# Kernel optimization log

Hardware: AMD Instinct MI355X
Metric: run time of the kernel (lower is better)

The kernel has to match this reference:

```python
import jax, jax.numpy as jnp
import numpy as np

BATCH, SEQ = 2, 2048
HID = 2048          # hidden_size
INTER = 4096        # intermediate_size
STATE = 16          # ssm_state_size
RANK = 128          # time_step_rank
K = 4               # conv_kernel


def setup_inputs() -> dict:
    key = jax.random.key(0)
    ks = jax.random.split(key, 8)
    s = 0.02
    return {
        "hidden_states": jax.random.normal(ks[0], (BATCH, SEQ, HID), jnp.float32),
        "in_proj_w": jax.random.normal(ks[1], (2 * INTER, HID), jnp.float32) * s,
        "conv_w": jax.random.normal(ks[2], (INTER, 1, K), jnp.float32) * s,   # depthwise (O, I/g=1, K)
        "conv_b": jnp.zeros((INTER,), jnp.float32),
        "x_proj_w": jax.random.normal(ks[3], (RANK + 2 * STATE, INTER), jnp.float32) * s,
        "dt_proj_w": jax.random.normal(ks[4], (INTER, RANK), jnp.float32) * s,
        "dt_proj_b": jax.random.normal(ks[5], (INTER,), jnp.float32) * s,
        "A_log": jnp.log(jnp.broadcast_to(jnp.arange(1, STATE + 1, dtype=jnp.float32), (INTER, STATE))),
        "D": jnp.ones((INTER,), jnp.float32),
        "out_proj_w": jax.random.normal(ks[6], (HID, INTER), jnp.float32) * s,
    }


def reference(hidden_states, in_proj_w, conv_w, conv_b, x_proj_w,
              dt_proj_w, dt_proj_b, A_log, D, out_proj_w):
    B, L, _ = hidden_states.shape
    # in_proj -> (B, L, 2*INTER), split into u (SSM input) and gate
    proj = jnp.einsum('blh,ph->blp', hidden_states, in_proj_w)
    u, gate = jnp.split(proj, 2, axis=-1)                       # (B, L, INTER) each
    # depthwise causal conv1d on channel-major layout (B, INTER, L)
    uc = jnp.swapaxes(u, 1, 2)
    conv = jax.lax.conv_general_dilated(
        uc, conv_w, window_strides=(1,), padding=[(K - 1, 0)],
        dimension_numbers=('NCH', 'OIH', 'NCH'), feature_group_count=INTER)
    u = jax.nn.silu(conv + conv_b[None, :, None])               # (B, INTER, L)
    # x_proj: dt-rank + B + C, computed in fp32 like the original
    ssm_p = jnp.einsum('bdl,pd->blp', u, x_proj_w).astype(jnp.float32)
    dt_r, Bm, Cm = jnp.split(ssm_p, [RANK, RANK + STATE], axis=-1)  # (B,L,RANK),(B,L,N),(B,L,N)
    dt = jax.nn.softplus(jnp.einsum('blr,dr->bld', dt_r, dt_proj_w) + dt_proj_b)  # (B, L, INTER)
    A = -jnp.exp(A_log)                                         # (INTER, STATE)

    def step(state, xs):
        dt_t, B_t, C_t, u_t = xs                                # (B,D),(B,N),(B,N),(B,D)
        dA = jnp.exp(dt_t[:, :, None] * A[None])                # (B, D, N)
        state = dA * state + (dt_t * u_t)[:, :, None] * B_t[:, None, :]
        y = jnp.einsum('bdn,bn->bd', state, C_t)
        return state, y

    xs = (jnp.swapaxes(dt, 0, 1),        # (L, B, D)
          jnp.swapaxes(Bm, 0, 1),        # (L, B, N)
          jnp.swapaxes(Cm, 0, 1),        # (L, B, N)
          jnp.moveaxis(u, 2, 0))         # (L, B, D)
    init = jnp.zeros((B, INTER, STATE), jnp.float32)
    _, ys = jax.lax.scan(step, init, xs)                        # (L, B, D)

    y = jnp.moveaxis(ys, 0, 1) + jnp.swapaxes(u, 1, 2) * D[None, None, :]  # skip connection
    y = y * jax.nn.silu(gate)
    return jnp.einsum('bld,hd->blh', y, out_proj_w)             # (B, L, HID)
```

## Files before the change

### kernel.cpp

```cpp
#include <hip/hip_runtime.h>

typedef unsigned int u32;
typedef unsigned short u16;
typedef float f32x4 __attribute__((ext_vector_type(4)));
typedef float f32x16 __attribute__((ext_vector_type(16)));
typedef u16 us4 __attribute__((ext_vector_type(4)));
typedef u16 us8 __attribute__((ext_vector_type(8)));
typedef __bf16 bf16x8 __attribute__((ext_vector_type(8)));

__device__ __forceinline__ u16 f2bf(float f) {
  u32 u = __builtin_bit_cast(u32, f);
  u += 0x7fffu + ((u >> 16) & 1u);
  return (u16)(u >> 16);
}
__device__ __forceinline__ float bf2f(u16 h) {
  u32 u = ((u32)h) << 16;
  return __builtin_bit_cast(float, u);
}
__device__ __forceinline__ void async16(const void* g, void* l) {
  __builtin_amdgcn_global_load_lds((const __attribute__((address_space(1))) void*)g,
                                   (__attribute__((address_space(3))) void*)l, 16, 0, 0);
}

template <int ACT, bool SPLITK = false>
__global__ __launch_bounds__(256) void gemm_bt(const u16* __restrict__ A,
                                               const u16* __restrict__ B,
                                               void* __restrict__ Cv,
                                               const float* __restrict__ bias,
                                               int K, int ldc) {
  __shared__ __align__(16) u16 As[128 * 64];
  __shared__ __align__(16) u16 Bs[128 * 64];
  const int tid = threadIdx.x;
  const int lane = tid & 63;
  const int wave = tid >> 6;
  const int ln = lane & 31;
  const int hw = lane >> 5;
  const int wm = (wave >> 1) << 6;
  const int wn = (wave & 1) << 6;
  const long rowBase = (long)blockIdx.y << 7;
  const long colBase = (long)blockIdx.x << 7;

  int kStart = 0, kEnd = K;
  if constexpr (SPLITK) {
    int kn = K / gridDim.z;
    kStart = blockIdx.z * kn;
    kEnd = kStart + kn;
  }

  const int rr = tid >> 3;
  const int qg = (tid & 7) ^ (rr & 7);
  const u16* Ag = A + (rowBase + rr) * (long)K + qg * 8;
  const u16* Bg = B + (colBase + rr) * (long)K + qg * 8;
  u16* Al = As + tid * 8;
  u16* Bl = Bs + tid * 8;

  f32x16 acc[2][2] = {};
  const int l7 = ln & 7;

  for (int k0 = kStart; k0 < kEnd; k0 += 64) {
#pragma unroll
    for (int c = 0; c < 4; ++c) {
      async16(Ag + 32L * c * K + k0, Al + 2048 * c);
      async16(Bg + 32L * c * K + k0, Bl + 2048 * c);
    }
    __syncthreads();
#pragma unroll
    for (int s = 0; s < 4; ++s) {
      const int xa = ((s * 2 + hw) ^ l7) * 8;
      us8 af[2], bfr[2];
#pragma unroll
      for (int i = 0; i < 2; ++i)
        af[i] = *(const us8*)(As + (wm + i * 32 + ln) * 64 + xa);
#pragma unroll
      for (int i = 0; i < 2; ++i)
        bfr[i] = *(const us8*)(Bs + (wn + i * 32 + ln) * 64 + xa);
#pragma unroll
      for (int i = 0; i < 2; ++i)
#pragma unroll
        for (int j = 0; j < 2; ++j)
          acc[i][j] = __builtin_amdgcn_mfma_f32_32x32x16_bf16(
              __builtin_bit_cast(bf16x8, af[i]), __builtin_bit_cast(bf16x8, bfr[j]),
              acc[i][j], 0, 0, 0);
    }
    __syncthreads();
  }

  float* Cf = (float*)Cv;
  if constexpr (SPLITK)
    Cf += (size_t)blockIdx.z * ((size_t)gridDim.y * 128 * ldc);

#pragma unroll
  for (int i = 0; i < 2; ++i)
#pragma unroll
    for (int j = 0; j < 2; ++j)
#pragma unroll
      for (int r = 0; r < 16; ++r) {
        long row = rowBase + wm + i * 32 + (r & 3) + 8 * (r >> 2) + 4 * hw;
        long col = colBase + wn + j * 32 + ln;
        float v = acc[i][j][r];
        if constexpr (ACT == 0) {
          Cf[row * ldc + col] = v;
        } else if constexpr (ACT == 1) {
          ((u16*)Cv)[row * ldc + col] = f2bf(v);
        } else if constexpr (ACT == 2) {
          float s = v / (1.f + __expf(-v));
          ((u16*)Cv)[row * ldc + col] = f2bf(s);
        } else if constexpr (ACT == 3) {
          v += bias[col];
          float sp = (v > 20.f) ? v : log1pf(__expf(v));
          Cf[row * ldc + col] = sp;
        } else if constexpr (ACT == 4) {
          v += bias[col];
          float sp = (v > 20.f) ? v : log1pf(__expf(v));
          ((u16*)Cv)[row * ldc + col] = f2bf(sp);
        } else {
          if (colBase < 4096) {
            ((u16*)Cv)[row * 4096 + col] = f2bf(v);
          } else {
            float s = v / (1.f + __expf(-v));
            ((u16*)(size_t)bias)[row * 4096 + (col - 4096)] = f2bf(s);
          }
        }
      }
}

__device__ __forceinline__ void cvt4(const float* __restrict__ in,
                                     u16* __restrict__ out, int i) {
  f32x4 v = ((const f32x4*)in)[i];
  us4 o;
  o[0] = f2bf(v[0]); o[1] = f2bf(v[1]); o[2] = f2bf(v[2]); o[3] = f2bf(v[3]);
  ((us4*)out)[i] = o;
}
__global__ __launch_bounds__(256) void cvt_all(
    const float* __restrict__ hs, const float* __restrict__ wIn,
    const float* __restrict__ wOut, const float* __restrict__ wDt,
    const float* __restrict__ wX, u16* __restrict__ Xb, u16* __restrict__ Winb,
    u16* __restrict__ Wob, u16* __restrict__ Wdtb, u16* __restrict__ Wxb) {
  int i = blockIdx.x * 256 + threadIdx.x;
  if (i < 2097152) { cvt4(hs, Xb, i); return; }
  i -= 2097152;
  if (i < 4194304) { cvt4(wIn, Winb, i); return; }
  i -= 4194304;
  if (i < 2097152) { cvt4(wOut, Wob, i); return; }
  i -= 2097152;
  if (i < 131072) { cvt4(wDt, Wdtb, i); return; }
  i -= 131072;
  if (i >= 262144) return;
  int row = (i << 2) >> 12;
  us4 o;
  if (row < 160) {
    f32x4 v = ((const f32x4*)wX)[i];
    o[0] = f2bf(v[0]); o[1] = f2bf(v[1]); o[2] = f2bf(v[2]); o[3] = f2bf(v[3]);
  } else {
    o[0] = 0; o[1] = 0; o[2] = 0; o[3] = 0;
  }
  ((us4*)Wxb)[i] = o;
}

__global__ __launch_bounds__(256) void xp_reduce(const float* __restrict__ part,
                                                 float* __restrict__ smp,
                                                 u16* __restrict__ dtrb) {
  int i = blockIdx.x * 256 + threadIdx.x;
  const f32x4* p = (const f32x4*)part;
  f32x4 v = p[i];
  v += p[i + 262144];
  v += p[i + 524288];
  v += p[i + 786432];
  ((f32x4*)smp)[i] = v;
  int e = i << 2;
  int c = e & 255;
  if (c < 128) {
    int t = e >> 8;
    us4 o;
    o[0] = f2bf(v[0]); o[1] = f2bf(v[1]); o[2] = f2bf(v[2]); o[3] = f2bf(v[3]);
    *(us4*)(dtrb + t * 128 + c) = o;
  }
}

__global__ __launch_bounds__(256) void conv_silu(const u16* __restrict__ U,
                                                 const float* __restrict__ cw,
                                                 const float* __restrict__ cb,
                                                 u16* __restrict__ out) {
  int i = blockIdx.x * 256 + threadIdx.x;
  int t = i >> 10;
  int d4 = (i & 1023) << 2;
  int l = t & 2047;
  float w[4][4];
#pragma unroll
  for (int j = 0; j < 4; ++j) {
    f32x4 wv = *(const f32x4*)(cw + (d4 + j) * 4);
    w[j][0] = wv[0]; w[j][1] = wv[1]; w[j][2] = wv[2]; w[j][3] = wv[3];
  }
  float r[4] = {cb[d4], cb[d4 + 1], cb[d4 + 2], cb[d4 + 3]};
#pragma unroll
  for (int k = 0; k < 4; ++k) {
    int ll = l - 3 + k;
    if (ll >= 0) {
      us4 xv = *(const us4*)(U + (size_t)(t - 3 + k) * 4096 + d4);
      r[0] += w[0][k] * bf2f(xv[0]);
      r[1] += w[1][k] * bf2f(xv[1]);
      r[2] += w[2][k] * bf2f(xv[2]);
      r[3] += w[3][k] * bf2f(xv[3]);
    }
  }
  us4 o;
#pragma unroll
  for (int j = 0; j < 4; ++j) {
    float v = r[j];
    float s = v / (1.f + __expf(-v));
    o[j] = f2bf(s);
  }
  *(us4*)(out + (size_t)t * 4096 + d4) = o;
}

__global__ __launch_bounds__(256) void scan_part(
    const u16* __restrict__ dt, const u16* __restrict__ ub,
    const float* __restrict__ ssmp, const float* __restrict__ Alog,
    float* __restrict__ Sout, float* __restrict__ dtsumo) {
  const int tid = threadIdx.x;
  const int chunk = blockIdx.x, dgrp = blockIdx.y, b = blockIdx.z;
  const int d = (dgrp << 8) + tid;
  float A[16];
#pragma unroll
  for (int q = 0; q < 4; ++q) {
    f32x4 v = *(const f32x4*)(Alog + d * 16 + q * 4);
    A[q * 4 + 0] = -__expf(v[0]);
    A[q * 4 + 1] = -__expf(v[1]);
    A[q * 4 + 2] = -__expf(v[2]);
    A[q * 4 + 3] = -__expf(v[3]);
  }
  bool fastl = true;
#pragma unroll
  for (int n = 1; n < 16; ++n)
    fastl = fastl && (fabsf(A[n] - (n + 1) * A[0]) <= 1e-4f * (float)(n + 1));
  const bool fast = (__ballot(fastl) == ~0ull);

  const int base = b * 2048 + chunk * 64;
  const u16* dtp = dt + (size_t)base * 4096 + d;
  const u16* up = ub + (size_t)base * 4096 + d;
  const float* Bp = ssmp + (size_t)base * 256 + 128;

  float s[16] = {};
  float dtsum = 0.f;
  float cdt[8], cu[8], ndt[8] = {}, nu[8] = {};
#pragma unroll
  for (int j = 0; j < 8; ++j) {
    cdt[j] = bf2f(dtp[j * 4096]);
    cu[j] = bf2f(up[j * 4096]);
  }
  for (int l0 = 0; l0 < 64; l0 += 8) {
    if (l0 + 8 < 64) {
      int o = (l0 + 8) * 4096;
#pragma unroll
      for (int j = 0; j < 8; ++j) {
        ndt[j] = bf2f(dtp[o + j * 4096]);
        nu[j] = bf2f(up[o + j * 4096]);
      }
    }
    if (fast) {
#pragma unroll
      for (int j = 0; j < 8; ++j) {
        float e1 = __expf(cdt[j] * A[0]);
        float x = cdt[j] * cu[j];
        const float* Bl = Bp + (l0 + j) * 256;
        f32x4 B0 = *(const f32x4*)(Bl);
        f32x4 B1 = *(const f32x4*)(Bl + 4);
        f32x4 B2 = *(const f32x4*)(Bl + 8);
        f32x4 B3 = *(const f32x4*)(Bl + 12);
        float p = 1.f;
#pragma unroll
        for (int n = 0; n < 16; ++n) {
          p *= e1;
          float Bn = (n < 4) ? B0[n & 3] : (n < 8) ? B1[n & 3] : (n < 12) ? B2[n & 3] : B3[n & 3];
          s[n] = fmaf(p, s[n], x * Bn);
        }
        dtsum += cdt[j];
      }
    } else {
#pragma unroll
      for (int j = 0; j < 8; ++j) {
        float x = cdt[j] * cu[j];
        const float* Bl = Bp + (l0 + j) * 256;
        f32x4 B0 = *(const f32x4*)(Bl);
        f32x4 B1 = *(const f32x4*)(Bl + 4);
        f32x4 B2 = *(const f32x4*)(Bl + 8);
        f32x4 B3 = *(const f32x4*)(Bl + 12);
#pragma unroll
        for (int n = 0; n < 16; ++n) {
          float e = __expf(cdt[j] * A[n]);
          float Bn = (n < 4) ? B0[n & 3] : (n < 8) ? B1[n & 3] : (n < 12) ? B2[n & 3] : B3[n & 3];
          s[n] = fmaf(e, s[n], x * Bn);
        }
        dtsum += cdt[j];
      }
    }
#pragma unroll
    for (int j = 0; j < 8; ++j) { cdt[j] = ndt[j]; cu[j] = nu[j]; }
  }
  size_t o = ((size_t)(b * 32 + chunk) * 16) * 4096 + d;
#pragma unroll
  for (int n = 0; n < 16; ++n) Sout[o + (size_t)n * 4096] = s[n];
  dtsumo[(size_t)(b * 32 + chunk) * 4096 + d] = dtsum;
}

__global__ __launch_bounds__(256) void scan_fold(
    const float* __restrict__ Sin, const float* __restrict__ dtsum,
    const float* __restrict__ Alog, float* __restrict__ Sinit) {
  const int tid = threadIdx.x;
  const int n = blockIdx.x, dgrp = blockIdx.y, b = blockIdx.z;
  const int d = (dgrp << 8) + tid;
  const float A = -__expf(Alog[d * 16 + n]);
  float run = 0.f;
  for (int c = 0; c < 32; ++c) {
    size_t o = ((size_t)(b * 32 + c) * 16 + n) * 4096 + d;
    Sinit[o] = run;
    float P = __expf(dtsum[(size_t)(b * 32 + c) * 4096 + d] * A);
    run = fmaf(P, run, Sin[o]);
  }
}

__global__ __launch_bounds__(256) void scan_y(
    const u16* __restrict__ dt, const u16* __restrict__ ub,
    const float* __restrict__ ssmp, const u16* __restrict__ gs,
    const float* __restrict__ Alog, const float* __restrict__ Dv,
    const float* __restrict__ Sinit, u16* __restrict__ yb) {
  const int tid = threadIdx.x;
  const int chunk = blockIdx.x, dgrp = blockIdx.y, b = blockIdx.z;
  const int d = (dgrp << 8) + tid;
  float A[16];
#pragma unroll
  for (int q = 0; q < 4; ++q) {
    f32x4 v = *(const f32x4*)(Alog + d * 16 + q * 4);
    A[q * 4 + 0] = -__expf(v[0]);
    A[q * 4 + 1] = -__expf(v[1]);
    A[q * 4 + 2] = -__expf(v[2]);
    A[q * 4 + 3] = -__expf(v[3]);
  }
  bool fastl = true;
#pragma unroll
  for (int n = 1; n < 16; ++n)
    fastl = fastl && (fabsf(A[n] - (n + 1) * A[0]) <= 1e-4f * (float)(n + 1));
  const bool fast = (__ballot(fastl) == ~0ull);
  const float Dd = Dv[d];

  const int base = b * 2048 + chunk * 64;
  const u16* dtp = dt + (size_t)base * 4096 + d;
  const u16* up = ub + (size_t)base * 4096 + d;
  const u16* gp = gs + (size_t)base * 4096 + d;
  const float* Bp = ssmp + (size_t)base * 256 + 128;
  u16* yo = yb + (size_t)base * 4096 + d;

  float s[16];
  {
    size_t o = ((size_t)(b * 32 + chunk) * 16) * 4096 + d;
#pragma unroll
    for (int n = 0; n < 16; ++n) s[n] = Sinit[o + (size_t)n * 4096];
  }

  float cdt[8], cu[8], cg[8], ndt[8] = {}, nu[8] = {}, ng[8] = {};
#pragma unroll
  for (int j = 0; j < 8; ++j) {
    cdt[j] = bf2f(dtp[j * 4096]);
    cu[j] = bf2f(up[j * 4096]);
    cg[j] = bf2f(gp[j * 4096]);
  }
  for (int l0 = 0; l0 < 64; l0 += 8) {
    if (l0 + 8 < 64) {
      int o = (l0 + 8) * 4096;
#pragma unroll
      for (int j = 0; j < 8; ++j) {
        ndt[j] = bf2f(dtp[o + j * 4096]);
        nu[j] = bf2f(up[o + j * 4096]);
        ng[j] = bf2f(gp[o + j * 4096]);
      }
    }
    if (fast) {
#pragma unroll
      for (int j = 0; j < 8; ++j) {
        float e1 = __expf(cdt[j] * A[0]);
        float x = cdt[j] * cu[j];
        const float* Bl = Bp + (l0 + j) * 256;
        f32x4 B0 = *(const f32x4*)(Bl);
        f32x4 B1 = *(const f32x4*)(Bl + 4);
        f32x4 B2 = *(const f32x4*)(Bl + 8);
        f32x4 B3 = *(const f32x4*)(Bl + 12);
        f32x4 C0 = *(const f32x4*)(Bl + 16);
        f32x4 C1 = *(const f32x4*)(Bl + 20);
        f32x4 C2 = *(const f32x4*)(Bl + 24);
        f32x4 C3 = *(const f32x4*)(Bl + 28);
        float p = 1.f;
        float y0 = 0.f, y1 = 0.f, y2 = 0.f, y3 = 0.f;
#pragma unroll
        for (int n = 0; n < 16; ++n) {
          p *= e1;
          float Bn = (n < 4) ? B0[n & 3] : (n < 8) ? B1[n & 3] : (n < 12) ? B2[n & 3] : B3[n & 3];
          float Cn = (n < 4) ? C0[n & 3] : (n < 8) ? C1[n & 3] : (n < 12) ? C2[n & 3] : C3[n & 3];
          s[n] = fmaf(p, s[n], x * Bn);
          if (n < 4) y0 = fmaf(s[n], Cn, y0);
          else if (n < 8) y1 = fmaf(s[n], Cn, y1);
          else if (n < 12) y2 = fmaf(s[n], Cn, y2);
          else y3 = fmaf(s[n], Cn, y3);
        }
        float y = (y0 + y1) + (y2 + y3);
        yo[(l0 + j) * 4096] = f2bf((y + cu[j] * Dd) * cg[j]);
      }
    } else {
#pragma unroll
      for (int j = 0; j < 8; ++j) {
        float x = cdt[j] * cu[j];
        const float* Bl = Bp + (l0 + j) * 256;
        f32x4 B0 = *(const f32x4*)(Bl);
        f32x4 B1 = *(const f32x4*)(Bl + 4);
        f32x4 B2 = *(const f32x4*)(Bl + 8);
        f32x4 B3 = *(const f32x4*)(Bl + 12);
        f32x4 C0 = *(const f32x4*)(Bl + 16);
        f32x4 C1 = *(const f32x4*)(Bl + 20);
        f32x4 C2 = *(const f32x4*)(Bl + 24);
        f32x4 C3 = *(const f32x4*)(Bl + 28);
        float y0 = 0.f, y1 = 0.f, y2 = 0.f, y3 = 0.f;
#pragma unroll
        for (int n = 0; n < 16; ++n) {
          float e = __expf(cdt[j] * A[n]);
          float Bn = (n < 4) ? B0[n & 3] : (n < 8) ? B1[n & 3] : (n < 12) ? B2[n & 3] : B3[n & 3];
          float Cn = (n < 4) ? C0[n & 3] : (n < 8) ? C1[n & 3] : (n < 12) ? C2[n & 3] : C3[n & 3];
          s[n] = fmaf(e, s[n], x * Bn);
          if (n < 4) y0 = fmaf(s[n], Cn, y0);
          else if (n < 8) y1 = fmaf(s[n], Cn, y1);
          else if (n < 12) y2 = fmaf(s[n], Cn, y2);
          else y3 = fmaf(s[n], Cn, y3);
        }
        float y = (y0 + y1) + (y2 + y3);
        yo[(l0 + j) * 4096] = f2bf((y + cu[j] * Dd) * cg[j]);
      }
    }
#pragma unroll
    for (int j = 0; j < 8; ++j) { cdt[j] = ndt[j]; cu[j] = nu[j]; cg[j] = ng[j]; }
  }
}

extern "C" void kernel_launch(void* const* d_in, const int* in_sizes, int n_in,
                              void* d_out, int out_size, void* d_ws,
                              size_t ws_size, hipStream_t stream) {
  (void)in_sizes; (void)n_in; (void)out_size; (void)ws_size;
  const float* hs = (const float*)d_in[0];
  const float* wIn = (const float*)d_in[1];
  const float* cw = (const float*)d_in[2];
  const float* cb = (const float*)d_in[3];
  const float* wX = (const float*)d_in[4];
  const float* wDt = (const float*)d_in[5];
  const float* bDt = (const float*)d_in[6];
  const float* Alog = (const float*)d_in[7];
  const float* Dv = (const float*)d_in[8];
  const float* wOut = (const float*)d_in[9];

  const size_t MB = 1ull << 20;
  char* w = (char*)d_ws;
  u16* Xb = (u16*)(w + 0 * MB);
  u16* Winb = (u16*)(w + 16 * MB);
  u16* Pu = (u16*)(w + 48 * MB);
  u16* Dtb = (u16*)(w + 0 * MB);
  u16* Yb = (u16*)(w + 64 * MB);
  u16* Ub = (u16*)(w + 96 * MB);
  u16* Wxb = (u16*)(w + 128 * MB);
  float* Smp = (float*)(w + 130 * MB);
  u16* Dtrb = (u16*)(w + 134 * MB);
  u16* Wdtb = (u16*)(w + 135 * MB);
  u16* Wob = (u16*)(w + 136 * MB);
  float* Schk = (float*)(w + 152 * MB);
  float* Xpart = (float*)(w + 152 * MB);
  float* Sinit = (float*)(w + 168 * MB);
  float* Dtsum = (float*)(w + 184 * MB);
  u16* Pg = (u16*)d_out;

  cvt_all<<<34304, 256, 0, stream>>>(hs, wIn, wOut, wDt, wX, Xb, Winb, Wob, Wdtb, Wxb);
  gemm_bt<5><<<dim3(64, 32), 256, 0, stream>>>(Xb, Winb, Pu, (const float*)Pg, 2048, 4096);
  conv_silu<<<16384, 256, 0, stream>>>(Pu, cw, cb, Ub);
  gemm_bt<0, true><<<dim3(2, 32, 4), 256, 0, stream>>>(Ub, Wxb, Xpart, nullptr, 4096, 256);
  xp_reduce<<<1024, 256, 0, stream>>>(Xpart, Smp, Dtrb);
  gemm_bt<4><<<dim3(32, 32), 256, 0, stream>>>(Dtrb, Wdtb, Dtb, bDt, 128, 4096);
  scan_part<<<dim3(32, 16, 2), 256, 0, stream>>>(Dtb, Ub, Smp, Alog, Schk, Dtsum);
  scan_fold<<<dim3(16, 16, 2), 256, 0, stream>>>(Schk, Dtsum, Alog, Sinit);
  scan_y<<<dim3(32, 16, 2), 256, 0, stream>>>(Dtb, Ub, Smp, Pg, Alog, Dv, Sinit, Yb);
  gemm_bt<0><<<dim3(16, 32), 256, 0, stream>>>(Yb, Wob, (float*)d_out, nullptr, 4096, 2048);
}
```

Baseline: 643.6 us.

## Replace in_proj GEMM with 256x256-tile pipelined MFMA kernel

Adds a new 512-thread GEMM kernel for the in_proj projection. It uses 256x256 output tiles, a multi-stage async global-to-LDS pipeline with swizzled LDS layout and manual vmcnt/barrier scheduling, 16x16x32 bf16 MFMA, and an XCD-aware block remap. The split u/gate SiLU epilogue is kept. The goal is to raise data reuse and overlap memory with compute for the largest GEMM, at the cost of complex hand-scheduled synchronisation that may be fragile and lower occupancy.

```diff
diff --git a/kernel.cpp b/kernel.cpp
--- a/kernel.cpp
+++ b/kernel.cpp
@@ -20,6 +20,131 @@
 __device__ __forceinline__ void async16(const void* g, void* l) {
   __builtin_amdgcn_global_load_lds((const __attribute__((address_space(1))) void*)g,
                                    (__attribute__((address_space(3))) void*)l, 16, 0, 0);
+}
+
+#define STG(GP, LP, OFF, KOFF)                              \
+  {                                                         \
+    async16((GP) + (KOFF), (LP) + (OFF));                   \
+    async16((GP) + 128L * K + (KOFF), (LP) + (OFF) + 4096); \
+  }
+
+#define PHASE(SET, KS, NH, STAGE_STMT, TAIL_STMT)                              \
+  {                                                                            \
+    const u16* Ap_ = As + (SET) * 16384 + (KS) * 8192;                         \
+    const u16* Bp_ = Bs + (SET) * 16384 + (KS) * 8192;                         \
+    if ((NH) == 0) {                                                           \
+      _Pragma("unroll") for (int mf = 0; mf < 8; ++mf)                         \
+          af[mf] = *(const us8*)(Ap_ + ra[mf]);                                \
+    }                                                                          \
+    us8 bq0 = *(const us8*)(Bp_ + rb[(NH) * 2]);                               \
+    us8 bq1 = *(const us8*)(Bp_ + rb[(NH) * 2 + 1]);                           \
+    STAGE_STMT;                                                                \
+    asm volatile("s_barrier" ::: "memory");                                    \
+    __builtin_amdgcn_s_setprio(1);                                             \
+    _Pragma("unroll") for (int mf = 0; mf < 8; ++mf) {                         \
+      acc[mf][(NH) * 2] = __builtin_amdgcn_mfma_f32_16x16x32_bf16(             \
+          __builtin_bit_cast(bf16x8, af[mf]), __builtin_bit_cast(bf16x8, bq0), \
+          acc[mf][(NH) * 2], 0, 0, 0);                                         \
+      acc[mf][(NH) * 2 + 1] = __builtin_amdgcn_mfma_f32_16x16x32_bf16(         \
+          __builtin_bit_cast(bf16x8, af[mf]), __builtin_bit_cast(bf16x8, bq1), \
+          acc[mf][(NH) * 2 + 1], 0, 0, 0);                                     \
+    }                                                                          \
+    __builtin_amdgcn_s_setprio(0);                                             \
+    TAIL_STMT;                                                                 \
+    asm volatile("s_barrier" ::: "memory");                                    \
+  }
+
+__global__ __launch_bounds__(512, 2) void gemm256(const u16* __restrict__ A,
+                                                  const u16* __restrict__ B,
+                                                  u16* __restrict__ U,
+                                                  u16* __restrict__ G, int K) {
+  __shared__ __align__(16) u16 As[32768];
+  __shared__ __align__(16) u16 Bs[32768];
+  const int tid = threadIdx.x;
+  const int lane = tid & 63;
+  const int wave = tid >> 6;
+  const int wm = wave >> 2;
+  const int wn = wave & 3;
+  const int l15 = lane & 15;
+  const int kc2 = lane >> 4;
+  const int pc2s = kc2 ^ ((l15 >> 1) & 3);
+
+  int nbx = (int)gridDim.x, nby = (int)gridDim.y;
+  int bid = (int)blockIdx.x * nby + (int)blockIdx.y;
+  int cpx = (nbx * nby) >> 3;
+  bid = (bid & 7) * cpx + (bid >> 3);
+  const long rowBase = (long)(bid % nby) << 8;
+  const long colBase = (long)(bid / nby) << 8;
+
+  const int c0 = ((tid & 3) ^ ((tid >> 3) & 3)) << 3;
+  const u16* Ag = A + (rowBase + (tid >> 2)) * (long)K + c0;
+  const u16* Bg = B + (colBase + (tid >> 2)) * (long)K + c0;
+  u16* Alds = As + tid * 8;
+  u16* Blds = Bs + tid * 8;
+
+  int ra[8], rb[4];
+#pragma unroll
+  for (int mf = 0; mf < 8; ++mf)
+    ra[mf] = (wm * 128 + mf * 16 + l15) * 32 + pc2s * 8;
+#pragma unroll
+  for (int nf = 0; nf < 4; ++nf)
+    rb[nf] = (wn * 64 + nf * 16 + l15) * 32 + pc2s * 8;
+
+  f32x4 acc[8][4] = {};
+  us8 af[8];
+
+  STG(Ag, Alds, 0, 0);
+  STG(Bg, Blds, 0, 0);
+  STG(Ag, Alds, 8192, 32);
+  STG(Bg, Blds, 8192, 32);
+  STG(Ag, Alds, 16384, 64);
+  STG(Bg, Blds, 16384, 64);
+  asm volatile("s_waitcnt vmcnt(4)" ::: "memory");
+  asm volatile("s_barrier" ::: "memory");
+
+  const int nIter = K >> 7;
+  for (int t = 0; t < nIter; ++t) {
+    const int k1 = (2 * t + 1) * 64;
+    const int k2 = (2 * t + 2) * 64;
+    const int k3 = (2 * t + 3) * 64;
+    const bool full = (t < nIter - 1);
+    PHASE(0, 0, 0, { STG(Ag, Alds, 24576, k1 + 32); }, {});
+    PHASE(0, 0, 1, { STG(Bg, Blds, 24576, k1 + 32); },
+          { asm volatile("s_waitcnt vmcnt(8)" ::: "memory"); });
+    PHASE(0, 1, 0, { if (full) STG(Ag, Alds, 0, k2); }, {});
+    PHASE(0, 1, 1, { if (full) STG(Bg, Blds, 0, k2); },
+          {
+            if (full) asm volatile("s_waitcnt vmcnt(8)" ::: "memory");
+            else asm volatile("s_waitcnt vmcnt(4)" ::: "memory");
+          });
+    PHASE(1, 0, 0, { if (full) STG(Ag, Alds, 8192, k2 + 32); }, {});
+    PHASE(1, 0, 1, { if (full) STG(Bg, Blds, 8192, k2 + 32); },
+          {
+            if (full) asm volatile("s_waitcnt vmcnt(8)" ::: "memory");
+            else asm volatile("s_waitcnt vmcnt(0)" ::: "memory");
+          });
+    PHASE(1, 1, 0, { if (full) STG(Ag, Alds, 16384, k3); }, {});
+    PHASE(1, 1, 1, { if (full) STG(Bg, Blds, 16384, k3); },
+          { if (full) asm volatile("s_waitcnt vmcnt(8)" ::: "memory"); });
+  }
+
+  const int gate = (colBase >= 4096);
+  u16* Out = gate ? G : U;
+  const long cb = gate ? (colBase - 4096) : colBase;
+#pragma unroll
+  for (int mf = 0; mf < 8; ++mf) {
+    long row0 = rowBase + wm * 128 + mf * 16 + (lane >> 4) * 4;
+#pragma unroll
+    for (int nf = 0; nf < 4; ++nf) {
+      long col = cb + wn * 64 + nf * 16 + l15;
+#pragma unroll
+      for (int r = 0; r < 4; ++r) {
+        float v = acc[mf][nf][r];
+        if (gate) v = v / (1.f + __expf(-v));
+        Out[(row0 + r) * 4096 + col] = f2bf(v);
+      }
+    }
+  }
 }
 
 template <int ACT, bool SPLITK = false>
@@ -100,11 +225,6 @@
         float v = acc[i][j][r];
         if constexpr (ACT == 0) {
           Cf[row * ldc + col] = v;
-        } else if constexpr (ACT == 1) {
-          ((u16*)Cv)[row * ldc + col] = f2bf(v);
-        } else if constexpr (ACT == 2) {
-          float s = v / (1.f + __expf(-v));
-          ((u16*)Cv)[row * ldc + col] = f2bf(s);
         } else if constexpr (ACT == 3) {
           v += bias[col];
           float sp = (v > 20.f) ? v : log1pf(__expf(v));
@@ -113,13 +233,6 @@
           v += bias[col];
           float sp = (v > 20.f) ? v : log1pf(__expf(v));
           ((u16*)Cv)[row * ldc + col] = f2bf(sp);
-        } else {
-          if (colBase < 4096) {
-            ((u16*)Cv)[row * 4096 + col] = f2bf(v);
-          } else {
-            float s = v / (1.f + __expf(-v));
-            ((u16*)(size_t)bias)[row * 4096 + (col - 4096)] = f2bf(s);
-          }
         }
       }
 }
@@ -473,7 +586,7 @@
   u16* Pg = (u16*)d_out;
 
   cvt_all<<<34304, 256, 0, stream>>>(hs, wIn, wOut, wDt, wX, Xb, Winb, Wob, Wdtb, Wxb);
-  gemm_bt<5><<<dim3(64, 32), 256, 0, stream>>>(Xb, Winb, Pu, (const float*)Pg, 2048, 4096);
+  gemm256<<<dim3(32, 16), 512, 0, stream>>>(Xb, Winb, Pu, Pg, 2048);
   conv_silu<<<16384, 256, 0, stream>>>(Pu, cw, cb, Ub);
   gemm_bt<0, true><<<dim3(2, 32, 4), 256, 0, stream>>>(Ub, Wxb, Xpart, nullptr, 4096, 256);
   xp_reduce<<<1024, 256, 0, stream>>>(Xpart, Smp, Dtrb);
```

New measurement: 788.9 us. 22.6% more time.
